# Kernel tuning notes

Measured on AMD Instinct MI355X. Metric: run time of the kernel, lower is better.

Reference implementation:

```python
import jax, jax.numpy as jnp
import numpy as np

HEADS = 12
HEAD_SIZE = 64
INF = 1e12  # K.infinity() in bert4keras

B, L, D = 8, 1024, 768


def setup_inputs() -> dict:
    key = jax.random.key(0)
    k1, k2 = jax.random.split(key)
    x = jax.random.normal(k1, (B, L, D), dtype=jnp.float32)
    W = jax.random.normal(k2, (D, HEADS * HEAD_SIZE * 2), dtype=jnp.float32) * (1.0 / np.sqrt(D))
    b = jnp.zeros((HEADS * HEAD_SIZE * 2,), dtype=jnp.float32)
    mask = jnp.ones((B, L), dtype=jnp.int32)
    return {"x": x, "W": W, "b": b, "mask": mask}


def _rope_sin_cos(seq_len, head_size, dtype):
    # SinusoidalPositionEmbedding(head_size, 'zero'):
    # emb[n, 2i] = sin(n * 10000^(-2i/S)), emb[n, 2i+1] = cos(...)
    pos = jnp.arange(seq_len, dtype=dtype)                       # [L]
    inv = jnp.power(jnp.asarray(10000.0, dtype),
                    -2.0 * jnp.arange(head_size // 2, dtype=dtype) / head_size)  # [S/2]
    ang = pos[:, None] * inv[None, :]                            # [L, S/2]
    # repeat_elements(..., 2, -1): [c0,c0,c1,c1,...]
    cos_pos = jnp.repeat(jnp.cos(ang), 2, axis=-1)               # [L, S]
    sin_pos = jnp.repeat(jnp.sin(ang), 2, axis=-1)               # [L, S]
    return sin_pos[None, :, None, :], cos_pos[None, :, None, :]  # [1,L,1,S]


def _rotate_half_interleaved(t):
    # stack([-t[...,1::2], t[...,::2]], -1).reshape(t.shape)
    t2 = jnp.stack([-t[..., 1::2], t[..., ::2]], axis=-1)
    return t2.reshape(t.shape)


def reference(x, W, b, mask):
    dtype = x.dtype
    Bq, Lq, _ = x.shape
    S = HEAD_SIZE
    # dense projection + head split: [B, L, H, 2S]
    proj = (jnp.einsum('bld,de->ble', x, W) + b).reshape(Bq, Lq, HEADS, 2 * S)
    qw, kw = proj[..., :S], proj[..., S:]
    # inline RoPE (interleaved variant)
    sin_pos, cos_pos = _rope_sin_cos(Lq, S, dtype)
    qw = qw * cos_pos + _rotate_half_interleaved(qw) * sin_pos
    kw = kw * cos_pos + _rotate_half_interleaved(kw) * sin_pos
    # bilinear score: [B, H, L, L]
    logits = jnp.einsum('bmhd,bnhd->bhmn', qw, kw)
    # padding mask on axis 2 (rows) and axis 3 (cols): x*m + (-INF)*(1-m)
    m = mask.astype(dtype)
    m_row = m[:, None, :, None]
    m_col = m[:, None, None, :]
    logits = logits * m_row + (-INF) * (1.0 - m_row)
    logits = logits * m_col + (-INF) * (1.0 - m_col)
    # upper-triangular (incl. diagonal) mask
    tri = jnp.triu(jnp.ones((Lq, Lq), dtype=dtype))
    logits = logits - (1.0 - tri) * INF
    return logits / np.sqrt(S).astype(np.float32)
```

## Files before the change

### kernel.cpp

```cpp
#include <hip/hip_runtime.h>
#include <hip/hip_bf16.h>
#include <stdint.h>

#define NHEADS 12
#define HS 64
#define NB 8
#define NL 1024
#define ND 768
#define NE 1536
#define INFV 1000000000000.0f

typedef __bf16 bf16x8 __attribute__((ext_vector_type(8)));
typedef float f32x4 __attribute__((ext_vector_type(4)));

typedef __attribute__((address_space(1))) const unsigned int gas_uint;
typedef __attribute__((address_space(3))) unsigned int las_uint;
#define GLOAD_LDS16(g, l) __builtin_amdgcn_global_load_lds((gas_uint*)(g), (las_uint*)(l), 16, 0, 0)

__device__ __forceinline__ unsigned short f2bf(float f) {
  unsigned int u = __builtin_bit_cast(unsigned int, f);
  u += 0x7fffu + ((u >> 16) & 1u);
  return (unsigned short)(u >> 16);
}

__device__ __forceinline__ bf16x8 load_frag(const unsigned short* p) {
  uint4 v = *(const uint4*)p;
  return __builtin_bit_cast(bf16x8, v);
}

__global__ __launch_bounds__(256) void k_prep(
    const float* __restrict__ x, const float* __restrict__ W,
    unsigned short* __restrict__ xb, unsigned short* __restrict__ wt,
    float* __restrict__ cst) {
  const int blk = blockIdx.x;
  if (blk < 6144) {
    int i = blk * 256 + threadIdx.x;
    float4 v = ((const float4*)x)[i];
    ushort4 o;
    o.x = f2bf(v.x); o.y = f2bf(v.y); o.z = f2bf(v.z); o.w = f2bf(v.w);
    ((ushort4*)xb)[i] = o;
  } else if (blk < 6144 + 288) {
    __shared__ float tile[64][65];
    int t = blk - 6144;
    int te = t % 24, td = t / 24;
    int c = threadIdx.x & 63, r4 = threadIdx.x >> 6;
    #pragma unroll
    for (int rr = 0; rr < 16; rr++) {
      int row = rr * 4 + r4;
      tile[row][c] = W[(size_t)(td * 64 + row) * NE + te * 64 + c];
    }
    __syncthreads();
    #pragma unroll
    for (int rr = 0; rr < 16; rr++) {
      int row = rr * 4 + r4;
      wt[(size_t)(te * 64 + row) * ND + td * 64 + c] = f2bf(tile[c][row]);
    }
  } else {
    int t = (blk - 6432) * 256 + threadIdx.x;
    int p = t >> 5, i = t & 31;
    float inv = powf(10000.0f, -(float)i / 32.0f);
    float sv, cv;
    sincosf((float)p * inv, &sv, &cv);
    cst[(p * 32 + i) * 2 + 0] = cv;
    cst[(p * 32 + i) * 2 + 1] = sv;
  }
}

__global__ __launch_bounds__(256, 4) void k_proj_fill(
    const unsigned short* __restrict__ xb,
    const unsigned short* __restrict__ wt,
    const float* __restrict__ bias,
    const float* __restrict__ cst,
    unsigned short* __restrict__ qbuf, unsigned short* __restrict__ kbuf,
    const int* __restrict__ mask, float* __restrict__ out) {
  const int tid = threadIdx.x;

  __shared__ char smem_b[32768];

  if (blockIdx.x >= 768) {
    const int e   = blockIdx.x - 768;
    const int bh  = e / 28;
    int u = e % 28;
    int tm = 1;
    #pragma unroll
    for (int k = 0; k < 6; k++) if (u >= tm) { u -= tm; tm++; }
    const int tn = u;
    const int b  = bh / NHEADS;
    const int* mrow = mask + b * NL;
    const int n0 = tn * 128 + (tid & 31) * 4;
    int4 mc = *(const int4*)&mrow[n0];
    float o0 = ((mc.x ? 0.0f : -INFV) - INFV) * 0.125f;
    float o1 = ((mc.y ? 0.0f : -INFV) - INFV) * 0.125f;
    float o2 = ((mc.z ? 0.0f : -INFV) - INFV) * 0.125f;
    float o3 = ((mc.w ? 0.0f : -INFV) - INFV) * 0.125f;
    const float oz = (-2.0f * INFV) * 0.125f;
    #pragma unroll
    for (int it = 0; it < 16; it++) {
      int m = tm * 128 + it * 8 + (tid >> 5);
      bool mr1 = (mrow[m] != 0);
      f32x4 o;
      o[0] = mr1 ? o0 : oz;
      o[1] = mr1 ? o1 : oz;
      o[2] = mr1 ? o2 : oz;
      o[3] = mr1 ? o3 : oz;
      __builtin_nontemporal_store(o, (f32x4*)(out + ((size_t)bh * NL + m) * NL + n0));
    }
    return;
  }

  const int blk = blockIdx.x;
  const int xcd = blk & 7;
  const int loc = blk >> 3;
  const int h   = loc % 12;
  const int mt  = xcd * 8 + loc / 12;
  const int m0  = mt * 128;
  const int e0  = h * 128;
  const int lane = tid & 63;
  const int w    = tid >> 6;
  const int wm = w >> 1, wn = w & 1;
  const int col_l = lane & 15, rq = lane >> 4;

  unsigned int goff[4];
  #pragma unroll
  for (int q = 0; q < 4; q++) {
    int p = q * 256 + tid;
    int r = p >> 3, sl = p & 7;
    goff[q] = r * ND + (sl ^ (r & 7)) * 8;
  }
  const unsigned short* gA = wt + (size_t)e0 * ND;
  const unsigned short* gB = xb + (size_t)m0 * ND;

  const int xr = col_l & 7;
  const unsigned int aRow = (unsigned)((wn * 64 + col_l) * 128);
  const unsigned int bRow = (unsigned)(16384 + (wm * 64 + col_l) * 128);

  f32x4 acc[4][4];
  #pragma unroll
  for (int i = 0; i < 4; i++)
    #pragma unroll
    for (int j = 0; j < 4; j++)
      #pragma unroll
      for (int q = 0; q < 4; q++) acc[i][j][q] = 0.0f;

  for (int kk = 0; kk < ND; kk += 64) {
    const unsigned short* sA = gA + kk;
    const unsigned short* sB = gB + kk;
    #pragma unroll
    for (int q = 0; q < 4; q++) GLOAD_LDS16(sA + goff[q], smem_b + (q * 256 + tid) * 16);
    #pragma unroll
    for (int q = 0; q < 4; q++) GLOAD_LDS16(sB + goff[q], smem_b + 16384 + (q * 256 + tid) * 16);
    __syncthreads();
    #pragma unroll
    for (int kkh = 0; kkh < 2; kkh++) {
      bf16x8 af[4], bfr[4];
      #pragma unroll
      for (int f = 0; f < 4; f++) {
        const unsigned int so = (((kkh << 2) | rq) ^ xr) * 16;
        af[f]  = __builtin_bit_cast(bf16x8, *(const uint4*)(smem_b + aRow + f * 2048 + so));
        bfr[f] = __builtin_bit_cast(bf16x8, *(const uint4*)(smem_b + bRow + f * 2048 + so));
      }
      #pragma unroll
      for (int i = 0; i < 4; i++)
        #pragma unroll
        for (int j = 0; j < 4; j++)
          acc[i][j] = __builtin_amdgcn_mfma_f32_16x16x32_bf16(af[i], bfr[j], acc[i][j], 0, 0, 0);
    }
    __syncthreads();
  }

  unsigned short* obuf = (wn == 1) ? kbuf : qbuf;
  #pragma unroll
  for (int j = 0; j < 4; j++) {
    const int m   = m0 + wm * 64 + j * 16 + col_l;
    const int pos = m & (NL - 1);
    const int bb  = m >> 10;
    const float* crow = cst + pos * 64;
    unsigned short* orow = obuf + (((size_t)(bb * NHEADS + h)) * NL + pos) * HS;
    #pragma unroll
    for (int i = 0; i < 4; i++) {
      const int s0 = i * 16 + rq * 4;
      float4 bv = *(const float4*)&bias[e0 + wn * 64 + s0];
      float4 tq = *(const float4*)(crow + s0);
      float v0 = acc[i][j][0] + bv.x;
      float v1 = acc[i][j][1] + bv.y;
      float v2 = acc[i][j][2] + bv.z;
      float v3 = acc[i][j][3] + bv.w;
      ushort4 o;
      o.x = f2bf(v0 * tq.x - v1 * tq.y);
      o.y = f2bf(v1 * tq.x + v0 * tq.y);
      o.z = f2bf(v2 * tq.z - v3 * tq.w);
      o.w = f2bf(v3 * tq.z + v2 * tq.w);
      *(ushort4*)&orow[s0] = o;
    }
  }
}

__global__ __launch_bounds__(256) void k_logits(
    const unsigned short* __restrict__ qbuf,
    const unsigned short* __restrict__ kbuf,
    const int* __restrict__ mask,
    float* __restrict__ out) {
  const int f  = blockIdx.x;
  const int r  = f & 7, t = f >> 3;
  const int bh = r + 8 * (t / 36);
  int u = t % 36;
  int tm = 0;
  #pragma unroll
  for (int k = 0; k < 7; k++) if (u >= 8 - tm) { u -= 8 - tm; tm++; }
  const int tn = tm + u;
  const int b  = bh / NHEADS;
  const int tid  = threadIdx.x;
  const int* mrow = mask + b * NL;

  const int lane = tid & 63;
  const int w    = tid >> 6;
  const int wm = w >> 1, wn = w & 1;
  const int m_base = tm * 128 + wm * 64;
  const int n_base = tn * 128 + wn * 64;
  const int col_l = lane & 15, rq = lane >> 4;
  const unsigned short* Q = qbuf + (size_t)bh * (NL * HS);
  const unsigned short* K = kbuf + (size_t)bh * (NL * HS);

  __shared__ float lds[64 * 132];

  f32x4 acc[4][4];
  #pragma unroll
  for (int i = 0; i < 4; i++)
    #pragma unroll
    for (int j = 0; j < 4; j++)
      #pragma unroll
      for (int q = 0; q < 4; q++) acc[i][j][q] = 0.0f;

  #pragma unroll
  for (int ks = 0; ks < 2; ks++) {
    bf16x8 ak[4], bq[4];
    #pragma unroll
    for (int ff = 0; ff < 4; ff++) {
      ak[ff] = load_frag(K + (size_t)(n_base + ff * 16 + col_l) * HS + ks * 32 + rq * 8);
      bq[ff] = load_frag(Q + (size_t)(m_base + ff * 16 + col_l) * HS + ks * 32 + rq * 8);
    }
    #pragma unroll
    for (int i = 0; i < 4; i++)
      #pragma unroll
      for (int j = 0; j < 4; j++)
        acc[i][j] = __builtin_amdgcn_mfma_f32_16x16x32_bf16(ak[i], bq[j], acc[i][j], 0, 0, 0);
  }

  const bool diag = (tn == tm);
  const int rb_row = tid >> 5;
  const int rb_c4  = (tid & 31) * 4;
  const int n_rb   = tn * 128 + rb_c4;
  int4 mc_rb = *(const int4*)&mrow[n_rb];
  const bool allmc = (mc_rb.x & mc_rb.y & mc_rb.z & mc_rb.w) != 0;

  #pragma unroll
  for (int pass = 0; pass < 2; pass++) {
    if (wm == pass) {
      #pragma unroll
      for (int j = 0; j < 4; j++) {
        const int rl = j * 16 + col_l;
        #pragma unroll
        for (int i = 0; i < 4; i++)
          *(f32x4*)&lds[rl * 132 + wn * 64 + i * 16 + rq * 4] = acc[i][j];
      }
    }
    __syncthreads();
    #pragma unroll
    for (int it = 0; it < 8; it++) {
      const int rl = it * 8 + rb_row;
      const int m  = tm * 128 + pass * 64 + rl;
      f32x4 v = *(const f32x4*)&lds[rl * 132 + rb_c4];
      if (mrow[m] == 0) { v[0] = -INFV; v[1] = -INFV; v[2] = -INFV; v[3] = -INFV; }
      if (!allmc) {
        if (mc_rb.x == 0) v[0] = -INFV;
        if (mc_rb.y == 0) v[1] = -INFV;
        if (mc_rb.z == 0) v[2] = -INFV;
        if (mc_rb.w == 0) v[3] = -INFV;
      }
      if (diag) {
        if (n_rb + 0 < m) v[0] -= INFV;
        if (n_rb + 1 < m) v[1] -= INFV;
        if (n_rb + 2 < m) v[2] -= INFV;
        if (n_rb + 3 < m) v[3] -= INFV;
      }
      v *= 0.125f;
      __builtin_nontemporal_store(v, (f32x4*)(out + ((size_t)bh * NL + m) * NL + n_rb));
    }
    __syncthreads();
  }
}

extern "C" void kernel_launch(void* const* d_in, const int* in_sizes, int n_in,
                              void* d_out, int out_size, void* d_ws, size_t ws_size,
                              hipStream_t stream) {
  const float* x    = (const float*)d_in[0];
  const float* W    = (const float*)d_in[1];
  const float* bias = (const float*)d_in[2];
  const int*   mask = (const int*)d_in[3];
  float* out = (float*)d_out;
  char* ws = (char*)d_ws;

  unsigned short* xb = (unsigned short*)(ws);
  unsigned short* wt = (unsigned short*)(ws + 12582912);
  unsigned short* qb = (unsigned short*)(ws + 14942208);
  unsigned short* kb = (unsigned short*)(ws + 27525120);
  float* cst = (float*)(ws + 40108032);

  k_prep<<<6560, 256, 0, stream>>>(x, W, xb, wt, cst);
  k_proj_fill<<<768 + 2688, 256, 0, stream>>>(xb, wt, bias, cst, qb, kb, mask, out);
  k_logits<<<3456, 256, 0, stream>>>(qb, kb, mask, out);
}
```

Measured before the change: 120.1 us.

## Fuse projection, fill and logits into one kernel with per-head flag sync

Merges the projection/fill kernel and the logits kernel into a single launch. Logits blocks spin on per-(batch,head) atomic counters that projection blocks increment with release semantics after writing Q/K. This removes a kernel boundary and lets the logits work overlap with the tail of the projection and the fill stores. It also swaps the padded LDS staging layout for an XOR-swizzled one and adds a memset of the flags. It relies on projection blocks being scheduled before the waiting blocks, since the spin-wait could deadlock if they were not.

```diff
diff --git a/kernel.cpp b/kernel.cpp
--- a/kernel.cpp
+++ b/kernel.cpp
@@ -66,24 +66,117 @@
   }
 }
 
-__global__ __launch_bounds__(256, 4) void k_proj_fill(
+__global__ __launch_bounds__(256, 4) void k_mega(
     const unsigned short* __restrict__ xb,
     const unsigned short* __restrict__ wt,
     const float* __restrict__ bias,
     const float* __restrict__ cst,
     unsigned short* __restrict__ qbuf, unsigned short* __restrict__ kbuf,
-    const int* __restrict__ mask, float* __restrict__ out) {
+    const int* __restrict__ mask, float* __restrict__ out,
+    int* __restrict__ flags) {
+  __shared__ char smem_b[32768];
   const int tid = threadIdx.x;
-
-  __shared__ char smem_b[32768];
-
-  if (blockIdx.x >= 768) {
-    const int e   = blockIdx.x - 768;
+  const int blk = blockIdx.x;
+
+  if (blk < 768) {
+    const int xcd = blk & 7;
+    const int loc = blk >> 3;
+    const int h   = loc % 12;
+    const int mt  = xcd * 8 + loc / 12;
+    const int m0  = mt * 128;
+    const int e0  = h * 128;
+    const int lane = tid & 63;
+    const int w    = tid >> 6;
+    const int wm = w >> 1, wn = w & 1;
+    const int col_l = lane & 15, rq = lane >> 4;
+
+    unsigned int goff[4];
+    #pragma unroll
+    for (int q = 0; q < 4; q++) {
+      int p = q * 256 + tid;
+      int r = p >> 3, sl = p & 7;
+      goff[q] = r * ND + (sl ^ (r & 7)) * 8;
+    }
+    const unsigned short* gA = wt + (size_t)e0 * ND;
+    const unsigned short* gB = xb + (size_t)m0 * ND;
+
+    const int xr = col_l & 7;
+    const unsigned int aRow = (unsigned)((wn * 64 + col_l) * 128);
+    const unsigned int bRow = (unsigned)(16384 + (wm * 64 + col_l) * 128);
+
+    f32x4 acc[4][4];
+    #pragma unroll
+    for (int i = 0; i < 4; i++)
+      #pragma unroll
+      for (int j = 0; j < 4; j++)
+        #pragma unroll
+        for (int q = 0; q < 4; q++) acc[i][j][q] = 0.0f;
+
+    for (int kk = 0; kk < ND; kk += 64) {
+      const unsigned short* sA = gA + kk;
+      const unsigned short* sB = gB + kk;
+      #pragma unroll
+      for (int q = 0; q < 4; q++) GLOAD_LDS16(sA + goff[q], smem_b + (q * 256 + tid) * 16);
+      #pragma unroll
+      for (int q = 0; q < 4; q++) GLOAD_LDS16(sB + goff[q], smem_b + 16384 + (q * 256 + tid) * 16);
+      __syncthreads();
+      #pragma unroll
+      for (int kkh = 0; kkh < 2; kkh++) {
+        bf16x8 af[4], bfr[4];
+        #pragma unroll
+        for (int f = 0; f < 4; f++) {
+          const unsigned int so = (((kkh << 2) | rq) ^ xr) * 16;
+          af[f]  = __builtin_bit_cast(bf16x8, *(const uint4*)(smem_b + aRow + f * 2048 + so));
+          bfr[f] = __builtin_bit_cast(bf16x8, *(const uint4*)(smem_b + bRow + f * 2048 + so));
+        }
+        #pragma unroll
+        for (int i = 0; i < 4; i++)
+          #pragma unroll
+          for (int j = 0; j < 4; j++)
+            acc[i][j] = __builtin_amdgcn_mfma_f32_16x16x32_bf16(af[i], bfr[j], acc[i][j], 0, 0, 0);
+      }
+      __syncthreads();
+    }
+
+    unsigned short* obuf = (wn == 1) ? kbuf : qbuf;
+    #pragma unroll
+    for (int j = 0; j < 4; j++) {
+      const int m   = m0 + wm * 64 + j * 16 + col_l;
+      const int pos = m & (NL - 1);
+      const int bb  = m >> 10;
+      const float* crow = cst + pos * 64;
+      unsigned short* orow = obuf + (((size_t)(bb * NHEADS + h)) * NL + pos) * HS;
+      #pragma unroll
+      for (int i = 0; i < 4; i++) {
+        const int s0 = i * 16 + rq * 4;
+        float4 bv = *(const float4*)&bias[e0 + wn * 64 + s0];
+        float4 tq = *(const float4*)(crow + s0);
+        float v0 = acc[i][j][0] + bv.x;
+        float v1 = acc[i][j][1] + bv.y;
+        float v2 = acc[i][j][2] + bv.z;
+        float v3 = acc[i][j][3] + bv.w;
+        ushort4 o;
+        o.x = f2bf(v0 * tq.x - v1 * tq.y);
+        o.y = f2bf(v1 * tq.x + v0 * tq.y);
+        o.z = f2bf(v2 * tq.z - v3 * tq.w);
+        o.w = f2bf(v3 * tq.z + v2 * tq.w);
+        *(ushort4*)&orow[s0] = o;
+      }
+    }
+    __syncthreads();
+    if (tid == 0)
+      __hip_atomic_fetch_add(&flags[(mt >> 3) * NHEADS + h], 1,
+                             __ATOMIC_RELEASE, __HIP_MEMORY_SCOPE_AGENT);
+    return;
+  }
+
+  if (blk < 3456) {
+    const int e   = blk - 768;
     const int bh  = e / 28;
     int u = e % 28;
     int tm = 1;
     #pragma unroll
-    for (int k = 0; k < 6; k++) if (u >= tm) { u -= tm; tm++; }
+    for (int kk = 0; kk < 6; kk++) if (u >= tm) { u -= tm; tm++; }
     const int tn = u;
     const int b  = bh / NHEADS;
     const int* mrow = mask + b * NL;
@@ -108,185 +201,104 @@
     return;
   }
 
-  const int blk = blockIdx.x;
-  const int xcd = blk & 7;
-  const int loc = blk >> 3;
-  const int h   = loc % 12;
-  const int mt  = xcd * 8 + loc / 12;
-  const int m0  = mt * 128;
-  const int e0  = h * 128;
-  const int lane = tid & 63;
-  const int w    = tid >> 6;
-  const int wm = w >> 1, wn = w & 1;
-  const int col_l = lane & 15, rq = lane >> 4;
-
-  unsigned int goff[4];
-  #pragma unroll
-  for (int q = 0; q < 4; q++) {
-    int p = q * 256 + tid;
-    int r = p >> 3, sl = p & 7;
-    goff[q] = r * ND + (sl ^ (r & 7)) * 8;
-  }
-  const unsigned short* gA = wt + (size_t)e0 * ND;
-  const unsigned short* gB = xb + (size_t)m0 * ND;
-
-  const int xr = col_l & 7;
-  const unsigned int aRow = (unsigned)((wn * 64 + col_l) * 128);
-  const unsigned int bRow = (unsigned)(16384 + (wm * 64 + col_l) * 128);
-
-  f32x4 acc[4][4];
-  #pragma unroll
-  for (int i = 0; i < 4; i++)
-    #pragma unroll
-    for (int j = 0; j < 4; j++)
-      #pragma unroll
-      for (int q = 0; q < 4; q++) acc[i][j][q] = 0.0f;
-
-  for (int kk = 0; kk < ND; kk += 64) {
-    const unsigned short* sA = gA + kk;
-    const unsigned short* sB = gB + kk;
-    #pragma unroll
-    for (int q = 0; q < 4; q++) GLOAD_LDS16(sA + goff[q], smem_b + (q * 256 + tid) * 16);
-    #pragma unroll
-    for (int q = 0; q < 4; q++) GLOAD_LDS16(sB + goff[q], smem_b + 16384 + (q * 256 + tid) * 16);
+  {
+    const int f  = blk - 3456;
+    const int r  = f & 7, t = f >> 3;
+    const int bh = r + 8 * (t / 36);
+    int u = t % 36;
+    int tm = 0;
+    #pragma unroll
+    for (int k = 0; k < 7; k++) if (u >= 8 - tm) { u -= 8 - tm; tm++; }
+    const int tn = tm + u;
+    const int b  = bh / NHEADS;
+    const int* mrow = mask + b * NL;
+
+    if (tid == 0) {
+      while (__hip_atomic_load(&flags[bh], __ATOMIC_ACQUIRE,
+                               __HIP_MEMORY_SCOPE_AGENT) < 8)
+        __builtin_amdgcn_s_sleep(8);
+    }
     __syncthreads();
-    #pragma unroll
-    for (int kkh = 0; kkh < 2; kkh++) {
-      bf16x8 af[4], bfr[4];
-      #pragma unroll
-      for (int f = 0; f < 4; f++) {
-        const unsigned int so = (((kkh << 2) | rq) ^ xr) * 16;
-        af[f]  = __builtin_bit_cast(bf16x8, *(const uint4*)(smem_b + aRow + f * 2048 + so));
-        bfr[f] = __builtin_bit_cast(bf16x8, *(const uint4*)(smem_b + bRow + f * 2048 + so));
+
+    const int lane = tid & 63;
+    const int w    = tid >> 6;
+    const int wm = w >> 1, wn = w & 1;
+    const int m_base = tm * 128 + wm * 64;
+    const int n_base = tn * 128 + wn * 64;
+    const int col_l = lane & 15, rq = lane >> 4;
+    const unsigned short* Q = qbuf + (size_t)bh * (NL * HS);
+    const unsigned short* K = kbuf + (size_t)bh * (NL * HS);
+    float* lds = (float*)smem_b;
+
+    f32x4 acc[4][4];
+    #pragma unroll
+    for (int i = 0; i < 4; i++)
+      #pragma unroll
+      for (int j = 0; j < 4; j++)
+        #pragma unroll
+        for (int q = 0; q < 4; q++) acc[i][j][q] = 0.0f;
+
+    #pragma unroll
+    for (int ks = 0; ks < 2; ks++) {
+      bf16x8 ak[4], bq[4];
+      #pragma unroll
+      for (int ff = 0; ff < 4; ff++) {
+        ak[ff] = load_frag(K + (size_t)(n_base + ff * 16 + col_l) * HS + ks * 32 + rq * 8);
+        bq[ff] = load_frag(Q + (size_t)(m_base + ff * 16 + col_l) * HS + ks * 32 + rq * 8);
       }
       #pragma unroll
       for (int i = 0; i < 4; i++)
         #pragma unroll
         for (int j = 0; j < 4; j++)
-          acc[i][j] = __builtin_amdgcn_mfma_f32_16x16x32_bf16(af[i], bfr[j], acc[i][j], 0, 0, 0);
-    }
-    __syncthreads();
-  }
-
-  unsigned short* obuf = (wn == 1) ? kbuf : qbuf;
-  #pragma unroll
-  for (int j = 0; j < 4; j++) {
-    const int m   = m0 + wm * 64 + j * 16 + col_l;
-    const int pos = m & (NL - 1);
-    const int bb  = m >> 10;
-    const float* crow = cst + pos * 64;
-    unsigned short* orow = obuf + (((size_t)(bb * NHEADS + h)) * NL + pos) * HS;
-    #pragma unroll
-    for (int i = 0; i < 4; i++) {
-      const int s0 = i * 16 + rq * 4;
-      float4 bv = *(const float4*)&bias[e0 + wn * 64 + s0];
-      float4 tq = *(const float4*)(crow + s0);
-      float v0 = acc[i][j][0] + bv.x;
-      float v1 = acc[i][j][1] + bv.y;
-      float v2 = acc[i][j][2] + bv.z;
-      float v3 = acc[i][j][3] + bv.w;
-      ushort4 o;
-      o.x = f2bf(v0 * tq.x - v1 * tq.y);
-      o.y = f2bf(v1 * tq.x + v0 * tq.y);
-      o.z = f2bf(v2 * tq.z - v3 * tq.w);
-      o.w = f2bf(v3 * tq.z + v2 * tq.w);
-      *(ushort4*)&orow[s0] = o;
-    }
-  }
-}
-
-__global__ __launch_bounds__(256) void k_logits(
-    const unsigned short* __restrict__ qbuf,
-    const unsigned short* __restrict__ kbuf,
-    const int* __restrict__ mask,
-    float* __restrict__ out) {
-  const int f  = blockIdx.x;
-  const int r  = f & 7, t = f >> 3;
-  const int bh = r + 8 * (t / 36);
-  int u = t % 36;
-  int tm = 0;
-  #pragma unroll
-  for (int k = 0; k < 7; k++) if (u >= 8 - tm) { u -= 8 - tm; tm++; }
-  const int tn = tm + u;
-  const int b  = bh / NHEADS;
-  const int tid  = threadIdx.x;
-  const int* mrow = mask + b * NL;
-
-  const int lane = tid & 63;
-  const int w    = tid >> 6;
-  const int wm = w >> 1, wn = w & 1;
-  const int m_base = tm * 128 + wm * 64;
-  const int n_base = tn * 128 + wn * 64;
-  const int col_l = lane & 15, rq = lane >> 4;
-  const unsigned short* Q = qbuf + (size_t)bh * (NL * HS);
-  const unsigned short* K = kbuf + (size_t)bh * (NL * HS);
-
-  __shared__ float lds[64 * 132];
-
-  f32x4 acc[4][4];
-  #pragma unroll
-  for (int i = 0; i < 4; i++)
-    #pragma unroll
-    for (int j = 0; j < 4; j++)
-      #pragma unroll
-      for (int q = 0; q < 4; q++) acc[i][j][q] = 0.0f;
-
-  #pragma unroll
-  for (int ks = 0; ks < 2; ks++) {
-    bf16x8 ak[4], bq[4];
-    #pragma unroll
-    for (int ff = 0; ff < 4; ff++) {
-      ak[ff] = load_frag(K + (size_t)(n_base + ff * 16 + col_l) * HS + ks * 32 + rq * 8);
-      bq[ff] = load_frag(Q + (size_t)(m_base + ff * 16 + col_l) * HS + ks * 32 + rq * 8);
-    }
-    #pragma unroll
-    for (int i = 0; i < 4; i++)
-      #pragma unroll
-      for (int j = 0; j < 4; j++)
-        acc[i][j] = __builtin_amdgcn_mfma_f32_16x16x32_bf16(ak[i], bq[j], acc[i][j], 0, 0, 0);
-  }
-
-  const bool diag = (tn == tm);
-  const int rb_row = tid >> 5;
-  const int rb_c4  = (tid & 31) * 4;
-  const int n_rb   = tn * 128 + rb_c4;
-  int4 mc_rb = *(const int4*)&mrow[n_rb];
-  const bool allmc = (mc_rb.x & mc_rb.y & mc_rb.z & mc_rb.w) != 0;
-
-  #pragma unroll
-  for (int pass = 0; pass < 2; pass++) {
-    if (wm == pass) {
-      #pragma unroll
-      for (int j = 0; j < 4; j++) {
-        const int rl = j * 16 + col_l;
-        #pragma unroll
-        for (int i = 0; i < 4; i++)
-          *(f32x4*)&lds[rl * 132 + wn * 64 + i * 16 + rq * 4] = acc[i][j];
-      }
-    }
-    __syncthreads();
-    #pragma unroll
-    for (int it = 0; it < 8; it++) {
-      const int rl = it * 8 + rb_row;
-      const int m  = tm * 128 + pass * 64 + rl;
-      f32x4 v = *(const f32x4*)&lds[rl * 132 + rb_c4];
-      if (mrow[m] == 0) { v[0] = -INFV; v[1] = -INFV; v[2] = -INFV; v[3] = -INFV; }
-      if (!allmc) {
-        if (mc_rb.x == 0) v[0] = -INFV;
-        if (mc_rb.y == 0) v[1] = -INFV;
-        if (mc_rb.z == 0) v[2] = -INFV;
-        if (mc_rb.w == 0) v[3] = -INFV;
-      }
-      if (diag) {
-        if (n_rb + 0 < m) v[0] -= INFV;
-        if (n_rb + 1 < m) v[1] -= INFV;
-        if (n_rb + 2 < m) v[2] -= INFV;
-        if (n_rb + 3 < m) v[3] -= INFV;
-      }
-      v *= 0.125f;
-      __builtin_nontemporal_store(v, (f32x4*)(out + ((size_t)bh * NL + m) * NL + n_rb));
-    }
-    __syncthreads();
+          acc[i][j] = __builtin_amdgcn_mfma_f32_16x16x32_bf16(ak[i], bq[j], acc[i][j], 0, 0, 0);
+    }
+
+    const bool diag = (tn == tm);
+    const int rb_row = tid >> 5;
+    const int rb_c4  = (tid & 31) * 4;
+    const int n_rb   = tn * 128 + rb_c4;
+    int4 mc_rb = *(const int4*)&mrow[n_rb];
+    const bool allmc = (mc_rb.x & mc_rb.y & mc_rb.z & mc_rb.w) != 0;
+
+    #pragma unroll
+    for (int pass = 0; pass < 2; pass++) {
+      if (wm == pass) {
+        #pragma unroll
+        for (int j = 0; j < 4; j++) {
+          const int rl = j * 16 + col_l;
+          const int sw = (rl & 7) << 2;
+          #pragma unroll
+          for (int i = 0; i < 4; i++) {
+            const int c = (wn * 64 + i * 16 + rq * 4) ^ sw;
+            *(f32x4*)&lds[rl * 128 + c] = acc[i][j];
+          }
+        }
+      }
+      __syncthreads();
+      #pragma unroll
+      for (int it = 0; it < 8; it++) {
+        const int rl = it * 8 + rb_row;
+        const int m  = tm * 128 + pass * 64 + rl;
+        const int c  = rb_c4 ^ ((rl & 7) << 2);
+        f32x4 v = *(const f32x4*)&lds[rl * 128 + c];
+        if (mrow[m] == 0) { v[0] = -INFV; v[1] = -INFV; v[2] = -INFV; v[3] = -INFV; }
+        if (!allmc) {
+          if (mc_rb.x == 0) v[0] = -INFV;
+          if (mc_rb.y == 0) v[1] = -INFV;
+          if (mc_rb.z == 0) v[2] = -INFV;
+          if (mc_rb.w == 0) v[3] = -INFV;
+        }
+        if (diag) {
+          if (n_rb + 0 < m) v[0] -= INFV;
+          if (n_rb + 1 < m) v[1] -= INFV;
+          if (n_rb + 2 < m) v[2] -= INFV;
+          if (n_rb + 3 < m) v[3] -= INFV;
+        }
+        v *= 0.125f;
+        __builtin_nontemporal_store(v, (f32x4*)(out + ((size_t)bh * NL + m) * NL + n_rb));
+      }
+      __syncthreads();
+    }
   }
 }
 
@@ -305,8 +317,9 @@
   unsigned short* qb = (unsigned short*)(ws + 14942208);
   unsigned short* kb = (unsigned short*)(ws + 27525120);
   float* cst = (float*)(ws + 40108032);
-
+  int* flags = (int*)(ws + 40370176);
+
+  hipMemsetAsync(flags, 0, 96 * sizeof(int), stream);
   k_prep<<<6560, 256, 0, stream>>>(x, W, xb, wt, cst);
-  k_proj_fill<<<768 + 2688, 256, 0, stream>>>(xb, wt, bias, cst, qb, kb, mask, out);
-  k_logits<<<3456, 256, 0, stream>>>(qb, kb, mask, out);
-}
+  k_mega<<<6912, 256, 0, stream>>>(xb, wt, bias, cst, qb, kb, mask, out, flags);
+}
```

New measurement: 165.0 us. +37.4%, slower.
